# Kernel tuning notes

Hardware: AMD Instinct MI355X
Metric: run time of the kernel (lower is better)

## Reference

```python
import jax, jax.numpy as jnp
import numpy as np

B, S, D, H = 128, 1024, 512, 512


def setup_inputs() -> dict:
    key = jax.random.key(0)
    ks = jax.random.split(key, 8)
    return {
        "input": jax.random.normal(ks[0], (B, D), jnp.float32),
        "context": jax.random.normal(ks[1], (B, S, D), jnp.float32),
        "mask": jax.random.randint(ks[2], (B, S), 0, 2).astype(bool),
        "W_in": jax.random.normal(ks[3], (H, D), jnp.float32) * (1.0 / np.sqrt(D)),
        "b_in": jax.random.normal(ks[4], (H,), jnp.float32) * 0.01,
        "W_ctx": jax.random.normal(ks[5], (H, D), jnp.float32) * (1.0 / np.sqrt(D)),
        "b_ctx": jax.random.normal(ks[6], (H,), jnp.float32) * 0.01,
        "V": jax.random.uniform(ks[7], (H,), jnp.float32, -1.0, 1.0),
    }


def reference(input, context, mask, W_in, b_in, W_ctx, b_ctx, V):
    # inp: [B, H] -> broadcast over S (torch: unsqueeze(2).expand)
    inp = input @ W_in.T + b_in
    # 1x1 Conv1d over permuted context == per-position linear: [B, H, S]
    ctx = jnp.einsum('bsd,hd->bhs', context, W_ctx) + b_ctx[None, :, None]
    # additive (Bahdanau) score: V . tanh(inp + ctx) over H -> [B, S]
    att = jnp.einsum('h,bhs->bs', V, jnp.tanh(inp[:, :, None] + ctx))
    att = jnp.where(mask, -jnp.inf, att)
    alpha = jax.nn.softmax(att, axis=-1)  # [B, S]
    # weighted sum of projected context: [B, H]
    hidden_state = jnp.einsum('bhs,bs->bh', ctx, alpha)
    return (hidden_state, alpha)
```

## Files before the change

kernel.cpp:

```cpp
#include <hip/hip_runtime.h>
#include <math.h>

#define B_ 128
#define S_ 1024
#define D_ 512
#define H_ 512

typedef _Float16 f16x4 __attribute__((ext_vector_type(4)));
typedef _Float16 f16x8 __attribute__((ext_vector_type(8)));
typedef float    f32x4 __attribute__((ext_vector_type(4)));

__global__ void zero_k(float* __restrict__ p, int n) {
    int i = blockIdx.x * 256 + threadIdx.x;
    if (i < n) p[i] = 0.f;
}

__global__ __launch_bounds__(256) void linear_k(const float* __restrict__ X,
                                                const float* __restrict__ W,
                                                const float* __restrict__ bias,
                                                float* __restrict__ out) {
    int idx = blockIdx.x * 256 + threadIdx.x;
    int b = idx >> 9;
    int h = idx & 511;
    const float4* x = (const float4*)(X + (size_t)b * D_);
    const float4* w = (const float4*)(W + (size_t)h * D_);
    float s = 0.f;
#pragma unroll 8
    for (int k = 0; k < D_ / 4; ++k) {
        float4 xv = x[k], wv = w[k];
        s = fmaf(xv.x, wv.x, s);
        s = fmaf(xv.y, wv.y, s);
        s = fmaf(xv.z, wv.z, s);
        s = fmaf(xv.w, wv.w, s);
    }
    out[idx] = s + bias[h];
}

__device__ inline f16x4 cvt4(float4 v) {
    f16x4 r;
    r[0] = (_Float16)v.x; r[1] = (_Float16)v.y;
    r[2] = (_Float16)v.z; r[3] = (_Float16)v.w;
    return r;
}

__device__ inline float fast_tanh(float x) {
    float e = __expf(2.f * x);
    return 1.f - 2.f / (e + 1.f);
}

__global__ __launch_bounds__(256) void score_mfma(const float* __restrict__ ctx,
                                                  const float* __restrict__ Wc,
                                                  const float* __restrict__ bc,
                                                  const float* __restrict__ Vv,
                                                  const float* __restrict__ inp,
                                                  float* __restrict__ att) {
    __shared__ __align__(16) _Float16 Ah[128][40];
    __shared__ __align__(16) _Float16 Bh[128][40];
    __shared__ float red[8][128];

    const int tid = threadIdx.x;
    const int h0 = blockIdx.x * 128;
    const int s0 = blockIdx.y * 128;
    const int b  = blockIdx.z;

    const int rb  = tid >> 3;
    const int grp = tid & 7;

    const int wave = tid >> 6;
    const int lane = tid & 63;
    const int wm = wave >> 1, wn = wave & 1;
    const int l15 = lane & 15, quad = lane >> 4;

    const float* Abase = Wc  + (size_t)(h0 + rb) * D_ + grp * 4;
    const float* Bbase = ctx + ((size_t)b * S_ + s0 + rb) * D_ + grp * 4;

    f32x4 acc[4][4];
#pragma unroll
    for (int mi = 0; mi < 4; ++mi)
#pragma unroll
        for (int ni = 0; ni < 4; ++ni) acc[mi][ni] = (f32x4){0.f, 0.f, 0.f, 0.f};

    float4 ra[4], rbv[4];
#pragma unroll
    for (int i = 0; i < 4; ++i) {
        ra[i]  = *(const float4*)(Abase + (size_t)(32 * i) * D_);
        rbv[i] = *(const float4*)(Bbase + (size_t)(32 * i) * D_);
    }

    for (int k0 = 0; k0 < D_; k0 += 32) {
        __syncthreads();
#pragma unroll
        for (int i = 0; i < 4; ++i) {
            const int row = rb + 32 * i;
            *(f16x4*)&Ah[row][grp * 4] = cvt4(ra[i]);
            *(f16x4*)&Bh[row][grp * 4] = cvt4(rbv[i]);
        }
        __syncthreads();
        if (k0 + 32 < D_) {
#pragma unroll
            for (int i = 0; i < 4; ++i) {
                ra[i]  = *(const float4*)(Abase + (size_t)(32 * i) * D_ + k0 + 32);
                rbv[i] = *(const float4*)(Bbase + (size_t)(32 * i) * D_ + k0 + 32);
            }
        }
        f16x8 bhf[4];
#pragma unroll
        for (int ni = 0; ni < 4; ++ni)
            bhf[ni] = *(const f16x8*)&Bh[wn * 64 + ni * 16 + l15][quad * 8];
#pragma unroll
        for (int mi = 0; mi < 4; ++mi) {
            f16x8 ah = *(const f16x8*)&Ah[wm * 64 + mi * 16 + l15][quad * 8];
#pragma unroll
            for (int ni = 0; ni < 4; ++ni)
                acc[mi][ni] = __builtin_amdgcn_mfma_f32_16x16x32_f16(ah, bhf[ni], acc[mi][ni], 0, 0, 0);
        }
    }

    float p[4] = {0.f, 0.f, 0.f, 0.f};
#pragma unroll
    for (int mi = 0; mi < 4; ++mi) {
#pragma unroll
        for (int r = 0; r < 4; ++r) {
            const int h = h0 + wm * 64 + mi * 16 + quad * 4 + r;
            const float c  = inp[(size_t)b * H_ + h] + bc[h];
            const float vh = Vv[h];
#pragma unroll
            for (int ni = 0; ni < 4; ++ni)
                p[ni] = fmaf(vh, fast_tanh(c + acc[mi][ni][r]), p[ni]);
        }
    }
    const int cid = wm * 4 + quad;
#pragma unroll
    for (int ni = 0; ni < 4; ++ni)
        red[cid][wn * 64 + ni * 16 + l15] = p[ni];
    __syncthreads();
    if (tid < 128) {
        float s = 0.f;
#pragma unroll
        for (int g = 0; g < 8; ++g) s += red[g][tid];
        atomicAdd(att + (size_t)b * S_ + s0 + tid, s);
    }
}

__global__ __launch_bounds__(256) void softmax_k(const float* __restrict__ att,
                                                 const int* __restrict__ mask,
                                                 float* __restrict__ alpha) {
    const int b = blockIdx.x;
    const int t = threadIdx.x;
    __shared__ float sm[256];
    float v[4];
    float mx = -INFINITY;
#pragma unroll
    for (int i = 0; i < 4; ++i) {
        int s = t + i * 256;
        float a = att[(size_t)b * S_ + s];
        int mk = mask[(size_t)b * S_ + s];
        v[i] = mk ? -INFINITY : a;
        mx = fmaxf(mx, v[i]);
    }
    sm[t] = mx;
    __syncthreads();
    for (int off = 128; off > 0; off >>= 1) {
        if (t < off) sm[t] = fmaxf(sm[t], sm[t + off]);
        __syncthreads();
    }
    mx = sm[0];
    __syncthreads();
    float e[4];
    float sum = 0.f;
#pragma unroll
    for (int i = 0; i < 4; ++i) {
        e[i] = expf(v[i] - mx);
        sum += e[i];
    }
    sm[t] = sum;
    __syncthreads();
    for (int off = 128; off > 0; off >>= 1) {
        if (t < off) sm[t] += sm[t + off];
        __syncthreads();
    }
    float inv = 1.f / sm[0];
#pragma unroll
    for (int i = 0; i < 4; ++i) alpha[(size_t)b * S_ + t + i * 256] = e[i] * inv;
}

__global__ __launch_bounds__(256) void cbar_k(const float* __restrict__ ctx,
                                              const float* __restrict__ alpha,
                                              float* __restrict__ cbar) {
    const int b = blockIdx.y;
    const int s0 = blockIdx.x * 128;
    const int t = threadIdx.x;
    const int c4 = t & 127;
    const int sh = t >> 7;
    __shared__ float al[128];
    __shared__ float4 red[128];
    if (t < 128) al[t] = alpha[(size_t)b * S_ + s0 + t];
    __syncthreads();
    const float4* base = (const float4*)(ctx + ((size_t)b * S_ + s0) * D_);
    float4 c = {0.f, 0.f, 0.f, 0.f};
#pragma unroll 4
    for (int s = sh; s < 128; s += 2) {
        float a = al[s];
        float4 x = base[(size_t)s * (D_ / 4) + c4];
        c.x = fmaf(a, x.x, c.x);
        c.y = fmaf(a, x.y, c.y);
        c.z = fmaf(a, x.z, c.z);
        c.w = fmaf(a, x.w, c.w);
    }
    if (sh == 1) red[c4] = c;
    __syncthreads();
    if (sh == 0) {
        float4 o = red[c4];
        float* dst = cbar + (size_t)b * D_ + c4 * 4;
        atomicAdd(dst + 0, c.x + o.x);
        atomicAdd(dst + 1, c.y + o.y);
        atomicAdd(dst + 2, c.z + o.z);
        atomicAdd(dst + 3, c.w + o.w);
    }
}

extern "C" void kernel_launch(void* const* d_in, const int* in_sizes, int n_in,
                              void* d_out, int out_size, void* d_ws, size_t ws_size,
                              hipStream_t stream) {
    const float* input = (const float*)d_in[0];
    const float* ctx   = (const float*)d_in[1];
    const int*   mask  = (const int*)d_in[2];
    const float* W_in  = (const float*)d_in[3];
    const float* b_in  = (const float*)d_in[4];
    const float* W_ctx = (const float*)d_in[5];
    const float* b_ctx = (const float*)d_in[6];
    const float* V     = (const float*)d_in[7];

    float* hidden = (float*)d_out;
    float* alpha  = (float*)d_out + B_ * H_;

    float* inp  = (float*)d_ws;
    float* att  = inp + B_ * H_;
    float* cbar = att + B_ * S_;

    int nz = B_ * S_ + B_ * D_;
    zero_k<<<(nz + 255) / 256, 256, 0, stream>>>(att, nz);

    linear_k<<<(B_ * H_) / 256, 256, 0, stream>>>(input, W_in, b_in, inp);

    dim3 g2(H_ / 128, S_ / 128, B_);
    score_mfma<<<g2, 256, 0, stream>>>(ctx, W_ctx, b_ctx, V, inp, att);

    softmax_k<<<B_, 256, 0, stream>>>(att, mask, alpha);

    dim3 g4(S_ / 128, B_);
    cbar_k<<<g4, 256, 0, stream>>>(ctx, alpha, cbar);

    linear_k<<<(B_ * H_) / 256, 256, 0, stream>>>(cbar, W_ctx, b_ctx, hidden);
}
```

Baseline: 587.7 us.

## Store projected context in fp16 and reduce it directly with alpha

When the workspace is large enough, the score kernel writes the projected context (B x S x H) to the workspace as fp16. The weighted sum then reads that buffer instead of re-reading fp32 context, and the final W_ctx linear is dropped by initializing hidden to the bias. The grid order also changes so s varies fastest. This trades the fp32 context re-read and the last GEMV for an extra fp16 write and read of the same size, and it depends on ws_size.

```diff
diff --git a/kernel.cpp b/kernel.cpp
--- a/kernel.cpp
+++ b/kernel.cpp
@@ -6,6 +6,7 @@
 #define D_ 512
 #define H_ 512
 
+typedef _Float16 f16x2 __attribute__((ext_vector_type(2)));
 typedef _Float16 f16x4 __attribute__((ext_vector_type(4)));
 typedef _Float16 f16x8 __attribute__((ext_vector_type(8)));
 typedef float    f32x4 __attribute__((ext_vector_type(4)));
@@ -13,6 +14,16 @@
 __global__ void zero_k(float* __restrict__ p, int n) {
     int i = blockIdx.x * 256 + threadIdx.x;
     if (i < n) p[i] = 0.f;
+}
+
+__global__ void init2_k(float* __restrict__ att, float* __restrict__ hidden,
+                        const float* __restrict__ bc) {
+    int i = blockIdx.x * 256 + threadIdx.x;
+    if (i < B_ * S_) att[i] = 0.f;
+    else if (i < B_ * S_ + B_ * H_) {
+        int j = i - B_ * S_;
+        hidden[j] = bc[j & (H_ - 1)];
+    }
 }
 
 __global__ __launch_bounds__(256) void linear_k(const float* __restrict__ X,
@@ -48,19 +59,21 @@
     return 1.f - 2.f / (e + 1.f);
 }
 
+template <bool WCTX>
 __global__ __launch_bounds__(256) void score_mfma(const float* __restrict__ ctx,
                                                   const float* __restrict__ Wc,
                                                   const float* __restrict__ bc,
                                                   const float* __restrict__ Vv,
                                                   const float* __restrict__ inp,
-                                                  float* __restrict__ att) {
+                                                  float* __restrict__ att,
+                                                  _Float16* __restrict__ ctxp) {
     __shared__ __align__(16) _Float16 Ah[128][40];
     __shared__ __align__(16) _Float16 Bh[128][40];
     __shared__ float red[8][128];
 
     const int tid = threadIdx.x;
-    const int h0 = blockIdx.x * 128;
-    const int s0 = blockIdx.y * 128;
+    const int s0 = blockIdx.x * 128;
+    const int h0 = blockIdx.y * 128;
     const int b  = blockIdx.z;
 
     const int rb  = tid >> 3;
@@ -113,6 +126,22 @@
 #pragma unroll
             for (int ni = 0; ni < 4; ++ni)
                 acc[mi][ni] = __builtin_amdgcn_mfma_f32_16x16x32_f16(ah, bhf[ni], acc[mi][ni], 0, 0, 0);
+        }
+    }
+
+    if (WCTX) {
+#pragma unroll
+        for (int ni = 0; ni < 4; ++ni) {
+            const size_t srow = ((size_t)b * S_ + s0 + wn * 64 + ni * 16 + l15) * H_;
+#pragma unroll
+            for (int mi = 0; mi < 4; ++mi) {
+                f16x4 v;
+                v[0] = (_Float16)acc[mi][ni][0];
+                v[1] = (_Float16)acc[mi][ni][1];
+                v[2] = (_Float16)acc[mi][ni][2];
+                v[3] = (_Float16)acc[mi][ni][3];
+                *(f16x4*)(ctxp + srow + h0 + wm * 64 + mi * 16 + quad * 4) = v;
+            }
         }
     }
 
@@ -182,6 +211,39 @@
     float inv = 1.f / sm[0];
 #pragma unroll
     for (int i = 0; i < 4; ++i) alpha[(size_t)b * S_ + t + i * 256] = e[i] * inv;
+}
+
+__global__ __launch_bounds__(256) void cbar2_k(const _Float16* __restrict__ ctxp,
+                                               const float* __restrict__ alpha,
+                                               float* __restrict__ hidden) {
+    const int b  = blockIdx.y;
+    const int s0 = blockIdx.x * 128;
+    const int t  = threadIdx.x;
+    const int w = t >> 6, lane = t & 63;
+    __shared__ float al[128];
+    __shared__ float red[3][512];
+    if (t < 128) al[t] = alpha[(size_t)b * S_ + s0 + t];
+    __syncthreads();
+    const _Float16* base = ctxp + ((size_t)b * S_ + s0) * H_ + lane * 8;
+    float acc[8] = {0.f, 0.f, 0.f, 0.f, 0.f, 0.f, 0.f, 0.f};
+#pragma unroll 4
+    for (int s = w; s < 128; s += 4) {
+        float a = al[s];
+        f16x8 v = *(const f16x8*)(base + (size_t)s * H_);
+#pragma unroll
+        for (int j = 0; j < 8; ++j) acc[j] = fmaf(a, (float)v[j], acc[j]);
+    }
+    if (w > 0) {
+#pragma unroll
+        for (int j = 0; j < 8; ++j) red[w - 1][lane * 8 + j] = acc[j];
+    }
+    __syncthreads();
+    if (w == 0) {
+        float* dst = hidden + (size_t)b * H_ + lane * 8;
+#pragma unroll
+        for (int j = 0; j < 8; ++j)
+            atomicAdd(dst + j, acc[j] + red[0][lane * 8 + j] + red[1][lane * 8 + j] + red[2][lane * 8 + j]);
+    }
 }
 
 __global__ __launch_bounds__(256) void cbar_k(const float* __restrict__ ctx,
@@ -237,19 +299,39 @@
     float* inp  = (float*)d_ws;
     float* att  = inp + B_ * H_;
     float* cbar = att + B_ * S_;
-
-    int nz = B_ * S_ + B_ * D_;
-    zero_k<<<(nz + 255) / 256, 256, 0, stream>>>(att, nz);
-
-    linear_k<<<(B_ * H_) / 256, 256, 0, stream>>>(input, W_in, b_in, inp);
-
-    dim3 g2(H_ / 128, S_ / 128, B_);
-    score_mfma<<<g2, 256, 0, stream>>>(ctx, W_ctx, b_ctx, V, inp, att);
-
-    softmax_k<<<B_, 256, 0, stream>>>(att, mask, alpha);
-
-    dim3 g4(S_ / 128, B_);
-    cbar_k<<<g4, 256, 0, stream>>>(ctx, alpha, cbar);
-
-    linear_k<<<(B_ * H_) / 256, 256, 0, stream>>>(cbar, W_ctx, b_ctx, hidden);
-}
+    _Float16* ctxp = (_Float16*)(cbar + B_ * D_);
+
+    const size_t base_bytes = (size_t)(B_ * H_ + B_ * S_ + B_ * D_) * sizeof(float);
+    const size_t ctxp_bytes = (size_t)B_ * S_ * H_ * sizeof(_Float16);
+    const bool big = ws_size >= base_bytes + ctxp_bytes;
+
+    dim3 g2(S_ / 128, H_ / 128, B_);
+
+    if (big) {
+        int ni = B_ * S_ + B_ * H_;
+        init2_k<<<(ni + 255) / 256, 256, 0, stream>>>(att, hidden, b_ctx);
+
+        linear_k<<<(B_ * H_) / 256, 256, 0, stream>>>(input, W_in, b_in, inp);
+
+        score_mfma<true><<<g2, 256, 0, stream>>>(ctx, W_ctx, b_ctx, V, inp, att, ctxp);
+
+        softmax_k<<<B_, 256, 0, stream>>>(att, mask, alpha);
+
+        dim3 g4(S_ / 128, B_);
+        cbar2_k<<<g4, 256, 0, stream>>>(ctxp, alpha, hidden);
+    } else {
+        int nz = B_ * S_ + B_ * D_;
+        zero_k<<<(nz + 255) / 256, 256, 0, stream>>>(att, nz);
+
+        linear_k<<<(B_ * H_) / 256, 256, 0, stream>>>(input, W_in, b_in, inp);
+
+        score_mfma<false><<<g2, 256, 0, stream>>>(ctx, W_ctx, b_ctx, V, inp, att, nullptr);
+
+        softmax_k<<<B_, 256, 0, stream>>>(att, mask, alpha);
+
+        dim3 g4(S_ / 128, B_);
+        cbar_k<<<g4, 256, 0, stream>>>(ctx, alpha, cbar);
+
+        linear_k<<<(B_ * H_) / 256, 256, 0, stream>>>(cbar, W_ctx, b_ctx, hidden);
+    }
+}
```

After: 567.6 us. 1.04x faster.
